# Kernel optimization log

Measured on AMD Instinct MI355X. Metric: run time of the kernel, lower is better.

Reference implementation:

```python
import jax, jax.numpy as jnp
import numpy as np

# --- constants from config ---
CU, CV, F, BASE = 257.446, 197.718, 387.777, 0.239965
INLIER_THRESHOLD = 0.5
ERROR_TOLERANCE = 0.5   # '3D'
NUM_ITERATIONS = 256
DIM = '3D'
BATCH, NPTS, NSAMP = 64, 16384, 6


def se3_inv(T):
    # T: ...x4x4 SE(3); inverse = [R^T, -R^T t]
    R = T[..., :3, :3]
    t = T[..., :3, 3:4]
    Rt = jnp.swapaxes(R, -1, -2)
    top = jnp.concatenate([Rt, -Rt @ t], axis=-1)
    bottom = jnp.broadcast_to(jnp.array([0.0, 0.0, 0.0, 1.0], T.dtype), top.shape[:-2] + (1, 4))
    return jnp.concatenate([top, bottom], axis=-2)


def weighted_svd_transform(src, trg, w):
    # src, trg: Bx4xS homogeneous points; w: Bx1xS weights. Returns T_trg_src (Bx4x4).
    ps, pt = src[:, :3, :], trg[:, :3, :]
    w_sum = jnp.sum(w, axis=2, keepdims=True)
    cs = jnp.sum(ps * w, axis=2, keepdims=True) / w_sum  # Bx3x1
    ct = jnp.sum(pt * w, axis=2, keepdims=True) / w_sum
    qs, qt = ps - cs, pt - ct
    cov = jnp.einsum('bis,bjs->bij', qt * w, qs)  # Bx3x3
    U, _, Vt = jnp.linalg.svd(cov)
    det = jnp.linalg.det(U @ Vt)
    diag = jnp.stack([jnp.ones_like(det), jnp.ones_like(det), det], axis=-1)  # Bx3
    R = jnp.einsum('bij,bj,bjk->bik', U, diag, Vt)
    t = ct - R @ cs
    top = jnp.concatenate([R, t], axis=2)
    bottom = jnp.broadcast_to(jnp.array([0.0, 0.0, 0.0, 1.0], src.dtype), (src.shape[0], 1, 4))
    return jnp.concatenate([top, bottom], axis=1)


def stereo_project(pts):
    # pts: Bx4xN homogeneous camera-frame points -> Bx4xN stereo image coords (ul, vl, ur, vr)
    M = jnp.array([[F, 0.0, CU, 0.0],
                   [0.0, F, CV, 0.0],
                   [F, 0.0, CU, -F * BASE],
                   [0.0, F, CV, 0.0]], pts.dtype)
    z = pts[:, 2:3, :]
    return jnp.einsum('ij,bjn->bin', M, pts) / z


def setup_inputs() -> dict:
    key = jax.random.key(0)
    ks = jax.random.split(key, 6)
    def homog(k):
        p = jax.random.normal(k, (BATCH, 3, NPTS), jnp.float32) * 5.0
        p = p.at[:, 2, :].set(jnp.abs(p[:, 2, :]) + 1.0)  # positive depth
        return jnp.concatenate([p, jnp.ones((BATCH, 1, NPTS), jnp.float32)], axis=1)
    keypoints_3D_src = homog(ks[0])
    keypoints_3D_trg = homog(ks[1])
    keypoints_2D_trg = jax.random.uniform(ks[2], (BATCH, 2, NPTS), jnp.float32) * 512.0
    valid_pts_src = jax.random.randint(ks[3], (BATCH, 1, NPTS), 0, 2).astype(jnp.int32)
    valid_pts_trg = jax.random.randint(ks[4], (BATCH, 1, NPTS), 0, 2).astype(jnp.int32)
    weights = jax.random.uniform(ks[5], (BATCH, 1, NPTS), jnp.float32, 1e-3, 1.0)
    # vehicle->sensor transform: small rotation about x + translation
    c, s = np.cos(0.1), np.sin(0.1)
    T_s_v = jnp.array([[1, 0, 0, 0.2], [0, c, -s, 0.0], [0, s, c, 1.0], [0, 0, 0, 1]], jnp.float32)
    return {'keypoints_3D_src': keypoints_3D_src, 'keypoints_3D_trg': keypoints_3D_trg,
            'keypoints_2D_trg': keypoints_2D_trg, 'valid_pts_src': valid_pts_src,
            'valid_pts_trg': valid_pts_trg, 'weights': weights, 'T_s_v': T_s_v}


def reference(keypoints_3D_src, keypoints_3D_trg, keypoints_2D_trg,
              valid_pts_src, valid_pts_trg, weights, T_s_v):
    B, _, N = keypoints_3D_src.shape
    pts_src = jax.lax.stop_gradient(keypoints_3D_src)
    pts_trg = jax.lax.stop_gradient(keypoints_3D_trg)
    pts2_trg = jax.lax.stop_gradient(keypoints_2D_trg)
    w = jax.lax.stop_gradient(weights)
    valid = (valid_pts_src[:, 0, :] > 0) & (valid_pts_trg[:, 0, :] > 0)  # BxN
    T_s_v_b = jnp.broadcast_to(T_s_v, (B, 4, 4))
    T_v_s_b = se3_inv(T_s_v_b)

    rand_idx = jax.random.randint(jax.random.key(42), (NUM_ITERATIONS, B, NSAMP), 0, N)

    def body(carry, idx):
        max_inl, inliers = carry
        idx4 = idx[:, None, :]
        s_src = jnp.take_along_axis(pts_src, jnp.broadcast_to(idx4, (B, 4, NSAMP)), axis=2)
        s_trg = jnp.take_along_axis(pts_trg, jnp.broadcast_to(idx4, (B, 4, NSAMP)), axis=2)
        s_w = jnp.take_along_axis(w, idx4, axis=2)
        T_trg_src = weighted_svd_transform(s_src, s_trg, s_w)          # Bx4x4
        T_cam = T_s_v_b @ T_trg_src @ T_v_s_b                          # Bx4x4
        est_3D = jnp.einsum('bij,bjn->bin', T_cam, pts_src)            # Bx4xN
        if DIM == '2D':
            est_2D = stereo_project(est_3D)[:, 0:2, :]
            err = jnp.linalg.norm(pts2_trg - est_2D, axis=1)
        else:
            err = jnp.linalg.norm(pts_trg[:, 0:3, :] - est_3D[:, 0:3, :], axis=1)
        small = (err < ERROR_TOLERANCE) & valid                        # BxN
        num = jnp.sum(small, axis=1).astype(jnp.int32)                 # B
        better = num > max_inl
        inliers = jnp.where(better[:, None], small, inliers)
        max_inl = jnp.where(better, num, max_inl)
        return (max_inl, inliers), None

    init = (jnp.zeros((B,), jnp.int32), jnp.zeros((B, N), bool))
    (_, inliers), _ = jax.lax.scan(body, init, rand_idx)
    return inliers.astype(jnp.float32)
```

## Files before the change

kernel.cpp:

```cpp
#include <hip/hip_runtime.h>
#include <stdint.h>
#include <math.h>

#define NPTS   16384
#define NBATCH 64
#define NITER  256
#define NSAMP  6
#define PPT    8
#define NCHUNK 8
#define ISPLIT 4
#define IPB    (NITER / ISPLIT)

__device__ __forceinline__ uint32_t rotl32(uint32_t v, uint32_t r) {
  return (v << r) | (v >> (32u - r));
}
__device__ __forceinline__ void tf_round(uint32_t& x0, uint32_t& x1, uint32_t r) {
  x0 += x1; x1 = rotl32(x1, r); x1 ^= x0;
}
__device__ void threefry2x32(uint32_t k0, uint32_t k1, uint32_t x0, uint32_t x1,
                             uint32_t& o0, uint32_t& o1) {
  uint32_t ks2 = k0 ^ k1 ^ 0x1BD11BDAu;
  x0 += k0; x1 += k1;
  tf_round(x0,x1,13); tf_round(x0,x1,15); tf_round(x0,x1,26); tf_round(x0,x1,6);
  x0 += k1; x1 += ks2 + 1u;
  tf_round(x0,x1,17); tf_round(x0,x1,29); tf_round(x0,x1,16); tf_round(x0,x1,24);
  x0 += ks2; x1 += k0 + 2u;
  tf_round(x0,x1,13); tf_round(x0,x1,15); tf_round(x0,x1,26); tf_round(x0,x1,6);
  x0 += k0; x1 += k1 + 3u;
  tf_round(x0,x1,17); tf_round(x0,x1,29); tf_round(x0,x1,16); tf_round(x0,x1,24);
  x0 += k1; x1 += ks2 + 4u;
  tf_round(x0,x1,13); tf_round(x0,x1,15); tf_round(x0,x1,26); tf_round(x0,x1,6);
  x0 += ks2; x1 += k0 + 5u;
  o0 = x0; o1 = x1;
}

template<int P, int Q>
__device__ __forceinline__ void jrot(double S[3][3], double V[3][3]) {
  double apq = S[P][Q];
  if (fabs(apq) > 1e-300) {
    double tau = (S[Q][Q] - S[P][P]) / (2.0 * apq);
    double t = copysign(1.0, tau) / (fabs(tau) + sqrt(1.0 + tau * tau));
    double c = 1.0 / sqrt(1.0 + t * t);
    double sn = t * c;
    #pragma unroll
    for (int k = 0; k < 3; ++k) {
      double skp = S[k][P], skq = S[k][Q];
      S[k][P] = c * skp - sn * skq;
      S[k][Q] = sn * skp + c * skq;
    }
    #pragma unroll
    for (int k = 0; k < 3; ++k) {
      double spk = S[P][k], sqk = S[Q][k];
      S[P][k] = c * spk - sn * sqk;
      S[Q][k] = sn * spk + c * sqk;
    }
    #pragma unroll
    for (int k = 0; k < 3; ++k) {
      double vkp = V[k][P], vkq = V[k][Q];
      V[k][P] = c * vkp - sn * vkq;
      V[k][Q] = sn * vkp + c * vkq;
    }
  }
}

__device__ __forceinline__ void swapd(double& a, double& b) { double t=a; a=b; b=t; }

__global__ __launch_bounds__(64) void fit_kernel(
    const float* __restrict__ src, const float* __restrict__ trg,
    const float* __restrict__ wts, const float* __restrict__ Tsv,
    float* __restrict__ models ,
    int* __restrict__ counts ) {
  const int b = blockIdx.x >> 2;
  const int iter = ((blockIdx.x & 3) << 6) | threadIdx.x;

  counts[b * NITER + iter] = 0;

  uint32_t K0, K1;
  threefry2x32(0u, 42u, 0u, 1u, K0, K1);

  const uint32_t base = (uint32_t)((iter * NBATCH + b) * NSAMP);
  int idx[NSAMP];
  #pragma unroll
  for (int s = 0; s < NSAMP; ++s) {
    uint32_t y0, y1;
    threefry2x32(K0, K1, 0u, base + (uint32_t)s, y0, y1);
    idx[s] = (int)((y0 ^ y1) & (uint32_t)(NPTS - 1));
  }

  const float* sb = src + (size_t)b * 4 * NPTS;
  const float* tb = trg + (size_t)b * 4 * NPTS;
  const float* wb = wts + (size_t)b * NPTS;

  float px[NSAMP], py[NSAMP], pz[NSAMP], qx[NSAMP], qy[NSAMP], qz[NSAMP], wv[NSAMP];
  #pragma unroll
  for (int s = 0; s < NSAMP; ++s) {
    int j = idx[s];
    px[s] = sb[j]; py[s] = sb[NPTS + j]; pz[s] = sb[2 * NPTS + j];
    qx[s] = tb[j]; qy[s] = tb[NPTS + j]; qz[s] = tb[2 * NPTS + j];
    wv[s] = wb[j];
  }

  double wsum = 0, csx = 0, csy = 0, csz = 0, ctx = 0, cty = 0, ctz = 0;
  #pragma unroll
  for (int s = 0; s < NSAMP; ++s) {
    double w = (double)wv[s];
    wsum += w;
    csx += (double)px[s] * w; csy += (double)py[s] * w; csz += (double)pz[s] * w;
    ctx += (double)qx[s] * w; cty += (double)qy[s] * w; ctz += (double)qz[s] * w;
  }
  double iw = 1.0 / wsum;
  csx *= iw; csy *= iw; csz *= iw; ctx *= iw; cty *= iw; ctz *= iw;

  double C00=0,C01=0,C02=0,C10=0,C11=0,C12=0,C20=0,C21=0,C22=0;
  #pragma unroll
  for (int s = 0; s < NSAMP; ++s) {
    double w = (double)wv[s];
    double ax = ((double)qx[s]-ctx)*w, ay = ((double)qy[s]-cty)*w, az = ((double)qz[s]-ctz)*w;
    double bx = (double)px[s]-csx, by = (double)py[s]-csy, bz = (double)pz[s]-csz;
    C00 += ax*bx; C01 += ax*by; C02 += ax*bz;
    C10 += ay*bx; C11 += ay*by; C12 += ay*bz;
    C20 += az*bx; C21 += az*by; C22 += az*bz;
  }

  double S[3][3], V[3][3] = {{1,0,0},{0,1,0},{0,0,1}};
  S[0][0] = C00*C00 + C10*C10 + C20*C20;
  S[0][1] = C00*C01 + C10*C11 + C20*C21;
  S[0][2] = C00*C02 + C10*C12 + C20*C22;
  S[1][1] = C01*C01 + C11*C11 + C21*C21;
  S[1][2] = C01*C02 + C11*C12 + C21*C22;
  S[2][2] = C02*C02 + C12*C12 + C22*C22;
  S[1][0] = S[0][1]; S[2][0] = S[0][2]; S[2][1] = S[1][2];
  #pragma unroll 1
  for (int sweep = 0; sweep < 6; ++sweep) {
    jrot<0,1>(S, V); jrot<0,2>(S, V); jrot<1,2>(S, V);
  }

  double l0 = S[0][0], l1 = S[1][1], l2 = S[2][2];
  double v0x=V[0][0], v0y=V[1][0], v0z=V[2][0];
  double v1x=V[0][1], v1y=V[1][1], v1z=V[2][1];
  double v2x=V[0][2], v2y=V[1][2], v2z=V[2][2];
  if (l0 < l1) { swapd(l0,l1); swapd(v0x,v1x); swapd(v0y,v1y); swapd(v0z,v1z); }
  if (l1 < l2) { swapd(l1,l2); swapd(v1x,v2x); swapd(v1y,v2y); swapd(v1z,v2z); }
  if (l0 < l1) { swapd(l0,l1); swapd(v0x,v1x); swapd(v0y,v1y); swapd(v0z,v1z); }

  double u0x = C00*v0x + C01*v0y + C02*v0z;
  double u0y = C10*v0x + C11*v0y + C12*v0z;
  double u0z = C20*v0x + C21*v0y + C22*v0z;
  double n0 = sqrt(u0x*u0x + u0y*u0y + u0z*u0z);
  double r0 = (n0 > 1e-150) ? 1.0 / n0 : 0.0;
  u0x *= r0; u0y *= r0; u0z *= r0;
  double u1x = C00*v1x + C01*v1y + C02*v1z;
  double u1y = C10*v1x + C11*v1y + C12*v1z;
  double u1z = C20*v1x + C21*v1y + C22*v1z;
  double d01 = u1x*u0x + u1y*u0y + u1z*u0z;
  u1x -= d01*u0x; u1y -= d01*u0y; u1z -= d01*u0z;
  double n1 = sqrt(u1x*u1x + u1y*u1y + u1z*u1z);
  double r1 = (n1 > 1e-150) ? 1.0 / n1 : 0.0;
  u1x *= r1; u1y *= r1; u1z *= r1;
  double u2x = u0y*u1z - u0z*u1y;
  double u2y = u0z*u1x - u0x*u1z;
  double u2z = u0x*u1y - u0y*u1x;
  double detV = v0x*(v1y*v2z - v1z*v2y) - v0y*(v1x*v2z - v1z*v2x) + v0z*(v1x*v2y - v1y*v2x);
  double R00 = u0x*v0x + u1x*v1x + detV*u2x*v2x;
  double R01 = u0x*v0y + u1x*v1y + detV*u2x*v2y;
  double R02 = u0x*v0z + u1x*v1z + detV*u2x*v2z;
  double R10 = u0y*v0x + u1y*v1x + detV*u2y*v2x;
  double R11 = u0y*v0y + u1y*v1y + detV*u2y*v2y;
  double R12 = u0y*v0z + u1y*v1z + detV*u2y*v2z;
  double R20 = u0z*v0x + u1z*v1x + detV*u2z*v2x;
  double R21 = u0z*v0y + u1z*v1y + detV*u2z*v2y;
  double R22 = u0z*v0z + u1z*v1z + detV*u2z*v2z;
  double tx = ctx - (R00*csx + R01*csy + R02*csz);
  double ty = cty - (R10*csx + R11*csy + R12*csz);
  double tz = ctz - (R20*csx + R21*csy + R22*csz);

  double A[4][4];
  #pragma unroll
  for (int i = 0; i < 4; ++i)
    #pragma unroll
    for (int j = 0; j < 4; ++j) A[i][j] = (double)Tsv[i*4 + j];
  double Tts[4][4] = {{R00,R01,R02,tx},{R10,R11,R12,ty},{R20,R21,R22,tz},{0,0,0,1}};
  double I[4][4];
  I[0][0]=A[0][0]; I[0][1]=A[1][0]; I[0][2]=A[2][0];
  I[1][0]=A[0][1]; I[1][1]=A[1][1]; I[1][2]=A[2][1];
  I[2][0]=A[0][2]; I[2][1]=A[1][2]; I[2][2]=A[2][2];
  I[0][3] = -(I[0][0]*A[0][3] + I[0][1]*A[1][3] + I[0][2]*A[2][3]);
  I[1][3] = -(I[1][0]*A[0][3] + I[1][1]*A[1][3] + I[1][2]*A[2][3]);
  I[2][3] = -(I[2][0]*A[0][3] + I[2][1]*A[1][3] + I[2][2]*A[2][3]);
  I[3][0]=0; I[3][1]=0; I[3][2]=0; I[3][3]=1;
  double M1[4][4];
  #pragma unroll
  for (int i = 0; i < 4; ++i)
    #pragma unroll
    for (int j = 0; j < 4; ++j)
      M1[i][j] = A[i][0]*Tts[0][j] + A[i][1]*Tts[1][j] + A[i][2]*Tts[2][j] + A[i][3]*Tts[3][j];
  float* mo = models + ((size_t)b * NITER + iter) * 12;
  #pragma unroll
  for (int i = 0; i < 3; ++i)
    #pragma unroll
    for (int j = 0; j < 4; ++j)
      mo[i*4 + j] = (float)(M1[i][0]*I[0][j] + M1[i][1]*I[1][j] + M1[i][2]*I[2][j] + M1[i][3]*I[3][j]);
}

__global__ __launch_bounds__(256) void count_kernel(
    const float* __restrict__ src, const float* __restrict__ trg,
    const int* __restrict__ vs, const int* __restrict__ vt,
    const float* __restrict__ models, int* __restrict__ counts) {
  __shared__ float M[IPB * 12];
  __shared__ int cl[IPB];
  const int b      = blockIdx.x >> 5;
  const int isplit = (blockIdx.x >> 3) & (ISPLIT - 1);
  const int chunk  = blockIdx.x & (NCHUNK - 1);
  const int ibase  = isplit * IPB;

  const float* mb = models + ((size_t)b * NITER + ibase) * 12;
  for (int i = threadIdx.x; i < IPB * 12; i += 256) M[i] = mb[i];
  if (threadIdx.x < IPB) cl[threadIdx.x] = 0;
  __syncthreads();

  const float* sb = src + (size_t)b * 4 * NPTS;
  const float* tb = trg + (size_t)b * 4 * NPTS;
  const int* vsb = vs + (size_t)b * NPTS;
  const int* vtb = vt + (size_t)b * NPTS;
  const int p0 = chunk * (256 * PPT) + threadIdx.x;

  float sx[PPT], sy[PPT], sz[PPT], tx[PPT], ty[PPT], tz[PPT];
  bool vd[PPT];
  #pragma unroll
  for (int k = 0; k < PPT; ++k) {
    int p = p0 + k * 256;
    sx[k] = sb[p]; sy[k] = sb[NPTS + p]; sz[k] = sb[2 * NPTS + p];
    tx[k] = tb[p]; ty[k] = tb[NPTS + p]; tz[k] = tb[2 * NPTS + p];
    vd[k] = (vsb[p] > 0) && (vtb[p] > 0);
  }

  float cur[12];
  #pragma unroll
  for (int j = 0; j < 12; ++j) cur[j] = M[j];

  #pragma unroll 2
  for (int it = 0; it < IPB; ++it) {
    const int nit = (it + 1 < IPB) ? it + 1 : it;
    float nxt[12];
    #pragma unroll
    for (int j = 0; j < 12; ++j) nxt[j] = M[nit * 12 + j];

    float m00=cur[0], m01=cur[1], m02=cur[2],  m03=cur[3];
    float m10=cur[4], m11=cur[5], m12=cur[6],  m13=cur[7];
    float m20=cur[8], m21=cur[9], m22=cur[10], m23=cur[11];
    int c = 0;
    #pragma unroll
    for (int k = 0; k < PPT; ++k) {
      float ex = fmaf(m00, sx[k], fmaf(m01, sy[k], fmaf(m02, sz[k], m03)));
      float ey = fmaf(m10, sx[k], fmaf(m11, sy[k], fmaf(m12, sz[k], m13)));
      float ez = fmaf(m20, sx[k], fmaf(m21, sy[k], fmaf(m22, sz[k], m23)));
      float dx = tx[k] - ex, dy = ty[k] - ey, dz = tz[k] - ez;
      float e2 = fmaf(dx, dx, fmaf(dy, dy, dz * dz));
      c += (e2 < 0.25f && vd[k]) ? 1 : 0;
    }
    c += __shfl_xor(c, 32); c += __shfl_xor(c, 16); c += __shfl_xor(c, 8);
    c += __shfl_xor(c, 4);  c += __shfl_xor(c, 2);  c += __shfl_xor(c, 1);
    if ((threadIdx.x & 63) == 0) atomicAdd(&cl[it], c);

    #pragma unroll
    for (int j = 0; j < 12; ++j) cur[j] = nxt[j];
  }
  __syncthreads();
  if (threadIdx.x < IPB)
    atomicAdd(&counts[(size_t)b * NITER + ibase + threadIdx.x], cl[threadIdx.x]);
}

__global__ __launch_bounds__(256) void output_kernel(
    const float* __restrict__ src, const float* __restrict__ trg,
    const int* __restrict__ vs, const int* __restrict__ vt,
    const float* __restrict__ models, const int* __restrict__ counts,
    float* __restrict__ out) {
  const int tid = blockIdx.x * 256 + threadIdx.x;
  const int b = tid >> 14;
  const int p = tid & (NPTS - 1);

  __shared__ int sbest[4];
  {
    int c = counts[b * NITER + threadIdx.x];
    int key = (c << 8) | (NITER - 1 - threadIdx.x);
    key = max(key, __shfl_xor(key, 32));
    key = max(key, __shfl_xor(key, 16));
    key = max(key, __shfl_xor(key, 8));
    key = max(key, __shfl_xor(key, 4));
    key = max(key, __shfl_xor(key, 2));
    key = max(key, __shfl_xor(key, 1));
    if ((threadIdx.x & 63) == 0) sbest[threadIdx.x >> 6] = key;
  }
  __syncthreads();
  const int best = max(max(sbest[0], sbest[1]), max(sbest[2], sbest[3]));
  const int it = (NITER - 1) - (best & 255);

  const float* m = models + ((size_t)b * NITER + it) * 12;
  float m00=m[0], m01=m[1], m02=m[2],  m03=m[3];
  float m10=m[4], m11=m[5], m12=m[6],  m13=m[7];
  float m20=m[8], m21=m[9], m22=m[10], m23=m[11];
  const float* sb = src + (size_t)b * 4 * NPTS;
  const float* tb = trg + (size_t)b * 4 * NPTS;
  float sxv = sb[p], syv = sb[NPTS + p], szv = sb[2 * NPTS + p];
  float txv = tb[p], tyv = tb[NPTS + p], tzv = tb[2 * NPTS + p];
  bool v = (vs[(size_t)b * NPTS + p] > 0) && (vt[(size_t)b * NPTS + p] > 0);
  float ex = fmaf(m00, sxv, fmaf(m01, syv, fmaf(m02, szv, m03)));
  float ey = fmaf(m10, sxv, fmaf(m11, syv, fmaf(m12, szv, m13)));
  float ez = fmaf(m20, sxv, fmaf(m21, syv, fmaf(m22, szv, m23)));
  float dx = txv - ex, dy = tyv - ey, dz = tzv - ez;
  float e2 = fmaf(dx, dx, fmaf(dy, dy, dz * dz));
  out[tid] = (e2 < 0.25f && v) ? 1.0f : 0.0f;
}

extern "C" void kernel_launch(void* const* d_in, const int* in_sizes, int n_in,
                              void* d_out, int out_size, void* d_ws, size_t ws_size,
                              hipStream_t stream) {
  (void)in_sizes; (void)n_in; (void)out_size; (void)ws_size;
  const float* src = (const float*)d_in[0];
  const float* trg = (const float*)d_in[1];
  const int*   vs  = (const int*)d_in[3];
  const int*   vt  = (const int*)d_in[4];
  const float* wts = (const float*)d_in[5];
  const float* Tsv = (const float*)d_in[6];
  float* out = (float*)d_out;

  char* ws = (char*)d_ws;
  float* models = (float*)ws;
  int* counts   = (int*)(ws + (size_t)NBATCH * NITER * 12 * 4);

  fit_kernel<<<NBATCH * 4, 64, 0, stream>>>(src, trg, wts, Tsv, models, counts);
  count_kernel<<<NBATCH * ISPLIT * NCHUNK, 256, 0, stream>>>(src, trg, vs, vt, models, counts);
  output_kernel<<<(NBATCH * NPTS) / 256, 256, 0, stream>>>(src, trg, vs, vt, models, counts, out);
}
```

Measured before the change: 215.1 us.

## Retile count kernel, pack paired iteration counts, fold validity into target sentinel

Each thread now holds 16 points instead of 8, so more model iterations are amortized per register-resident point set; the grid splits iterations 8 ways and points 4 ways. Models are read from LDS as float4 rows. Validity is folded into a huge sentinel x-coordinate on the target, which removes a per-point select. Two iterations are processed per loop step, and their counts are packed into one 32-bit value so a single shuffle reduction serves both. The cost is higher register pressure from the doubled per-thread point arrays, which may reduce occupancy. The packing relies on per-wave counts staying below 65536.

```diff
diff --git a/kernel.cpp b/kernel.cpp
--- a/kernel.cpp
+++ b/kernel.cpp
@@ -6,9 +6,9 @@
 #define NBATCH 64
 #define NITER  256
 #define NSAMP  6
-#define PPT    8
-#define NCHUNK 8
-#define ISPLIT 4
+#define PPT    16
+#define NCHUNK 4
+#define ISPLIT 8
 #define IPB    (NITER / ISPLIT)
 
 __device__ __forceinline__ uint32_t rotl32(uint32_t v, uint32_t r) {
@@ -206,15 +206,15 @@
     const float* __restrict__ src, const float* __restrict__ trg,
     const int* __restrict__ vs, const int* __restrict__ vt,
     const float* __restrict__ models, int* __restrict__ counts) {
-  __shared__ float M[IPB * 12];
+  __shared__ float4 M4[IPB * 3];
   __shared__ int cl[IPB];
   const int b      = blockIdx.x >> 5;
-  const int isplit = (blockIdx.x >> 3) & (ISPLIT - 1);
+  const int isplit = (blockIdx.x >> 2) & (ISPLIT - 1);
   const int chunk  = blockIdx.x & (NCHUNK - 1);
   const int ibase  = isplit * IPB;
 
-  const float* mb = models + ((size_t)b * NITER + ibase) * 12;
-  for (int i = threadIdx.x; i < IPB * 12; i += 256) M[i] = mb[i];
+  const float4* mb4 = (const float4*)(models + ((size_t)b * NITER + ibase) * 12);
+  for (int i = threadIdx.x; i < IPB * 3; i += 256) M4[i] = mb4[i];
   if (threadIdx.x < IPB) cl[threadIdx.x] = 0;
   __syncthreads();
 
@@ -225,45 +225,44 @@
   const int p0 = chunk * (256 * PPT) + threadIdx.x;
 
   float sx[PPT], sy[PPT], sz[PPT], tx[PPT], ty[PPT], tz[PPT];
-  bool vd[PPT];
   #pragma unroll
   for (int k = 0; k < PPT; ++k) {
     int p = p0 + k * 256;
+    bool vd = (vsb[p] > 0) && (vtb[p] > 0);
     sx[k] = sb[p]; sy[k] = sb[NPTS + p]; sz[k] = sb[2 * NPTS + p];
-    tx[k] = tb[p]; ty[k] = tb[NPTS + p]; tz[k] = tb[2 * NPTS + p];
-    vd[k] = (vsb[p] > 0) && (vtb[p] > 0);
-  }
-
-  float cur[12];
-  #pragma unroll
-  for (int j = 0; j < 12; ++j) cur[j] = M[j];
-
-  #pragma unroll 2
-  for (int it = 0; it < IPB; ++it) {
-    const int nit = (it + 1 < IPB) ? it + 1 : it;
-    float nxt[12];
-    #pragma unroll
-    for (int j = 0; j < 12; ++j) nxt[j] = M[nit * 12 + j];
-
-    float m00=cur[0], m01=cur[1], m02=cur[2],  m03=cur[3];
-    float m10=cur[4], m11=cur[5], m12=cur[6],  m13=cur[7];
-    float m20=cur[8], m21=cur[9], m22=cur[10], m23=cur[11];
-    int c = 0;
+    tx[k] = vd ? tb[p] : 3.0e38f;
+    ty[k] = tb[NPTS + p]; tz[k] = tb[2 * NPTS + p];
+  }
+
+  for (int it = 0; it < IPB; it += 2) {
+    float4 r0 = M4[it * 3 + 0], r1 = M4[it * 3 + 1], r2 = M4[it * 3 + 2];
+    int c0 = 0;
     #pragma unroll
     for (int k = 0; k < PPT; ++k) {
-      float ex = fmaf(m00, sx[k], fmaf(m01, sy[k], fmaf(m02, sz[k], m03)));
-      float ey = fmaf(m10, sx[k], fmaf(m11, sy[k], fmaf(m12, sz[k], m13)));
-      float ez = fmaf(m20, sx[k], fmaf(m21, sy[k], fmaf(m22, sz[k], m23)));
+      float ex = fmaf(r0.x, sx[k], fmaf(r0.y, sy[k], fmaf(r0.z, sz[k], r0.w)));
+      float ey = fmaf(r1.x, sx[k], fmaf(r1.y, sy[k], fmaf(r1.z, sz[k], r1.w)));
+      float ez = fmaf(r2.x, sx[k], fmaf(r2.y, sy[k], fmaf(r2.z, sz[k], r2.w)));
       float dx = tx[k] - ex, dy = ty[k] - ey, dz = tz[k] - ez;
       float e2 = fmaf(dx, dx, fmaf(dy, dy, dz * dz));
-      c += (e2 < 0.25f && vd[k]) ? 1 : 0;
-    }
-    c += __shfl_xor(c, 32); c += __shfl_xor(c, 16); c += __shfl_xor(c, 8);
-    c += __shfl_xor(c, 4);  c += __shfl_xor(c, 2);  c += __shfl_xor(c, 1);
-    if ((threadIdx.x & 63) == 0) atomicAdd(&cl[it], c);
-
-    #pragma unroll
-    for (int j = 0; j < 12; ++j) cur[j] = nxt[j];
+      c0 += (e2 < 0.25f) ? 1 : 0;
+    }
+    float4 q0 = M4[it * 3 + 3], q1 = M4[it * 3 + 4], q2 = M4[it * 3 + 5];
+    int c1 = 0;
+    #pragma unroll
+    for (int k = 0; k < PPT; ++k) {
+      float ex = fmaf(q0.x, sx[k], fmaf(q0.y, sy[k], fmaf(q0.z, sz[k], q0.w)));
+      float ey = fmaf(q1.x, sx[k], fmaf(q1.y, sy[k], fmaf(q1.z, sz[k], q1.w)));
+      float ez = fmaf(q2.x, sx[k], fmaf(q2.y, sy[k], fmaf(q2.z, sz[k], q2.w)));
+      float dx = tx[k] - ex, dy = ty[k] - ey, dz = tz[k] - ez;
+      float e2 = fmaf(dx, dx, fmaf(dy, dy, dz * dz));
+      c1 += (e2 < 0.25f) ? 1 : 0;
+    }
+    unsigned s = (unsigned)c0 | ((unsigned)c1 << 16);
+    s += __shfl_xor(s, 32); s += __shfl_xor(s, 16); s += __shfl_xor(s, 8);
+    s += __shfl_xor(s, 4);  s += __shfl_xor(s, 2);  s += __shfl_xor(s, 1);
+    const int lane = threadIdx.x & 63;
+    if (lane == 0)      atomicAdd(&cl[it],     (int)(s & 0xffffu));
+    else if (lane == 1) atomicAdd(&cl[it + 1], (int)(s >> 16));
   }
   __syncthreads();
   if (threadIdx.x < IPB)
```

Measured after the change: 216.9 us. About the same (+0.8%).
